# Kernel tuning notes

Hardware: AMD Instinct MI355X
Metric: run time of the kernel (lower is better)

## Reference

```python
import jax, jax.numpy as jnp
import numpy as np

B, T, D, DIM = 32, 2048, 1024, 1024


def setup_inputs() -> dict:
    key = jax.random.key(0)
    ks = jax.random.split(key, 7)
    def glorot(k, shape):
        lim = np.sqrt(6.0 / (shape[0] + shape[1]))
        return jax.random.uniform(k, shape, jnp.float32, -lim, lim)
    return {
        "input_states": jax.random.normal(ks[0], (B, T, D), jnp.float32),
        "last_state": jax.random.normal(ks[1], (B, D), jnp.float32),
        "Wy": glorot(ks[2], (D, DIM)),
        "Wh": glorot(ks[3], (D, DIM)),
        "w": glorot(ks[4], (DIM, 1)),
        "Wp": glorot(ks[5], (D, DIM)),
        "Wx": glorot(ks[6], (D, DIM)),
    }


def reference(input_states, last_state, Wy, Wh, w, Wp, Wx):
    # hs: (B,T,dim); last_state projection broadcast over T (the original
    # tiles last_state via a ones-matmul; a plain broadcast is the same math)
    hs = jnp.einsum("btd,de->bte", input_states, Wy)
    hproj = last_state @ Wh                      # (B,dim)
    m = jax.nn.relu(hs + hproj[:, None, :])      # (B,T,dim)
    scores = jnp.einsum("bte,eo->bt", m, w[:, :1])  # squeeze last dim
    alpha = jax.nn.softmax(scores, axis=-1)      # (B,T)
    r = jnp.einsum("bt,btd->bd", alpha, input_states)
    out = jax.nn.relu(r @ Wp + last_state @ Wx)  # (B,dim)
    return out
```

## Files before the change

kernel.cpp:

```cpp
#include <hip/hip_runtime.h>
#include <hip/hip_bf16.h>
#include <stdint.h>

#define BB 32
#define TT 2048
#define DD 1024
#define DIMQ 1024
#define MTOT (BB*TT)

typedef __attribute__((ext_vector_type(8))) __bf16 bf16x8;
typedef __attribute__((ext_vector_type(4))) float f32x4;

__device__ __forceinline__ unsigned short f2bf(float f) {
    unsigned int u = __float_as_uint(f);
    u += 0x7FFF + ((u >> 16) & 1);
    return (unsigned short)(u >> 16);
}
__device__ __forceinline__ float bf2f(unsigned short s) {
    return __uint_as_float(((unsigned int)s) << 16);
}

__device__ __forceinline__ void load_lds16(const void* g, void* l) {
    __builtin_amdgcn_global_load_lds(
        (const __attribute__((address_space(1))) unsigned int*)g,
        (__attribute__((address_space(3))) unsigned int*)l,
        16, 0, 0);
}

__global__ void cast_x(const float* __restrict__ x, unsigned short* __restrict__ xb) {
    long i = ((long)blockIdx.x * blockDim.x + threadIdx.x) * 4;
    float4 a = *(const float4*)(x + i);
    ushort4 o;
    o.x = f2bf(a.x); o.y = f2bf(a.y); o.z = f2bf(a.z); o.w = f2bf(a.w);
    *(ushort4*)(xb + i) = o;
}

__global__ void transpose_cast(const float* __restrict__ Wsrc, unsigned short* __restrict__ Wdst) {
    __shared__ float tile[32][33];
    int bx = blockIdx.x * 32;
    int by = blockIdx.y * 32;
    int tx = threadIdx.x & 31;
    int ty4 = (threadIdx.x >> 5) * 4;
    #pragma unroll
    for (int r = 0; r < 4; r++)
        tile[ty4 + r][tx] = Wsrc[(size_t)(by + ty4 + r) * DIMQ + bx + tx];
    __syncthreads();
    #pragma unroll
    for (int r = 0; r < 4; r++)
        Wdst[(size_t)(bx + ty4 + r) * DD + by + tx] = f2bf(tile[tx][ty4 + r]);
}

__global__ void vecmat2(const float* __restrict__ last,
                        const float* __restrict__ Wh, const float* __restrict__ Wx,
                        float* __restrict__ hproj, float* __restrict__ lsWx) {
    __shared__ float vs[DD];
    __shared__ float red[4][64];
    int b = blockIdx.y;
    int e0 = blockIdx.x * 64;
    const float* Mat = blockIdx.z ? Wx : Wh;
    float* outp = blockIdx.z ? lsWx : hproj;
    int tid = threadIdx.x;
    for (int d = tid; d < DD; d += 256) vs[d] = last[b * DD + d];
    __syncthreads();
    int e = tid & 63, dg = tid >> 6;
    int d0 = dg * 256;
    const float* Mp = Mat + (size_t)d0 * DIMQ + e0 + e;
    float acc = 0.f;
    #pragma unroll 8
    for (int d = 0; d < 256; d++) acc += vs[d0 + d] * Mp[(size_t)d * DIMQ];
    red[dg][e] = acc;
    __syncthreads();
    if (dg == 0)
        outp[b * DIMQ + e0 + e] = red[0][e] + red[1][e] + red[2][e] + red[3][e];
}

__global__ __launch_bounds__(512, 2)
void gemm_scores(const unsigned short* __restrict__ Xb,
                 const unsigned short* __restrict__ WyT,
                 const float* __restrict__ hproj,
                 const float* __restrict__ wvec,
                 float* __restrict__ partials) {
    __shared__ unsigned short lds[65536];
    __shared__ float lp[256];

    int tid = threadIdx.x;
    int lane = tid & 63;
    int wave = tid >> 6;
    int wr = wave >> 2;
    int wc = wave & 3;

    int bidx = blockIdx.x;
    int rr = bidx & 255, rnd = bidx >> 8;
    int xcd = rr & 7, slot = rr >> 3;
    int ntile = slot & 3;
    int mtile = rnd * 64 + xcd * 8 + (slot >> 2);

    if (tid < 256) lp[tid] = 0.f;

    int ssub = wave >> 1, sks = wave & 1;
    const unsigned short* aG = Xb  + (size_t)(mtile * 256 + ssub * 16 + (lane & 15)) * DD + sks * 32 + (lane >> 4) * 8;
    const unsigned short* bG = WyT + (size_t)(ntile * 256 + ssub * 16 + (lane & 15)) * DD + sks * 32 + (lane >> 4) * 8;
    unsigned short* ldsAst = &lds[(ssub * 128 + sks * 64 + lane) * 8];
    unsigned short* ldsBst = ldsAst + 16384;

    const unsigned short* aRd = &lds[wr * 8192 + lane * 8];
    const unsigned short* bRd = &lds[16384 + (wc >> 1) * 8192 + (wc & 1) * 4096 + lane * 8];

#define STAGE_A(S_, H_, T_) { \
    const unsigned short* g_ = aG + (size_t)(H_) * 131072 + (T_) * 64; \
    load_lds16(g_,         ldsAst + (S_) * 32768 + (H_) * 8192);       \
    load_lds16(g_ + 65536, ldsAst + (S_) * 32768 + (H_) * 8192 + 4096); }
#define STAGE_B(S_, H_, T_) { \
    const unsigned short* g_ = bG + (size_t)(H_) * 131072 + (T_) * 64; \
    load_lds16(g_,         ldsBst + (S_) * 32768 + (H_) * 8192);       \
    load_lds16(g_ + 65536, ldsBst + (S_) * 32768 + (H_) * 8192 + 4096); }
#define STAGE_TILE(S_, T_) { STAGE_A(S_, 0, T_); STAGE_A(S_, 1, T_); \
                             STAGE_B(S_, 0, T_); STAGE_B(S_, 1, T_); }

    f32x4 acc[8][4] = {};
    bf16x8 af[4][2], bfr[4][2];

#define LDA(S_, MH) { \
    _Pragma("unroll") for (int i_ = 0; i_ < 4; i_++) \
    _Pragma("unroll") for (int k_ = 0; k_ < 2; k_++) \
        af[i_][k_] = *reinterpret_cast<const bf16x8*>(aRd + (S_) * 32768 + ((MH) * 4 + i_) * 1024 + k_ * 512); }
#define LDB(S_, NH) { \
    _Pragma("unroll") for (int j_ = 0; j_ < 2; j_++) \
    _Pragma("unroll") for (int k_ = 0; k_ < 2; k_++) \
        bfr[(NH) * 2 + j_][k_] = *reinterpret_cast<const bf16x8*>(bRd + (S_) * 32768 + ((NH) * 2 + j_) * 1024 + k_ * 512); }
#define MFMA_Q(MH, NH) { \
    _Pragma("unroll") for (int k_ = 0; k_ < 2; k_++) \
    _Pragma("unroll") for (int i_ = 0; i_ < 4; i_++) \
    _Pragma("unroll") for (int j_ = 0; j_ < 2; j_++) \
        acc[(MH) * 4 + i_][(NH) * 2 + j_] = __builtin_amdgcn_mfma_f32_16x16x32_bf16( \
            af[i_][k_], bfr[(NH) * 2 + j_][k_], acc[(MH) * 4 + i_][(NH) * 2 + j_], 0, 0, 0); }

#define BAR() __builtin_amdgcn_s_barrier()
#define LGKM0() asm volatile("s_waitcnt lgkmcnt(0)" ::: "memory")
#define VMW8() asm volatile("s_waitcnt vmcnt(8)" ::: "memory")
#define PRIO1() __builtin_amdgcn_s_setprio(1)
#define PRIO0() __builtin_amdgcn_s_setprio(0)

    STAGE_TILE(0, 0);
    STAGE_TILE(1, 1);

    #pragma unroll 2
    for (int t = 0; t < 16; ++t) {
        int s = t & 1;
        int tp = (t + 2 > 15) ? 15 : (t + 2);

        VMW8();
        BAR();

        LDB(s, 0); LDB(s, 1);
        LDA(s, 0);
        PRIO1(); MFMA_Q(0, 0); MFMA_Q(0, 1); PRIO0();

        LDA(s, 1);
        LGKM0();
        BAR();

        STAGE_TILE(s, tp);
        PRIO1(); MFMA_Q(1, 0); MFMA_Q(1, 1); PRIO0();
    }

    __syncthreads();

    int bIdx = mtile >> 3;
    int q = lane >> 4, l15 = lane & 15;

    float hpv[4], wvv[4];
    #pragma unroll
    for (int nf = 0; nf < 4; nf++) {
        int n = ntile * 256 + wc * 64 + nf * 16 + l15;
        hpv[nf] = hproj[bIdx * DIMQ + n];
        wvv[nf] = wvec[n];
    }

    #pragma unroll
    for (int m = 0; m < 8; m++) {
        f32x4 s = {0.f, 0.f, 0.f, 0.f};
        #pragma unroll
        for (int nf = 0; nf < 4; nf++) {
            #pragma unroll
            for (int r = 0; r < 4; r++) {
                float v = acc[m][nf][r] + hpv[nf];
                v = v > 0.f ? v : 0.f;
                s[r] += v * wvv[nf];
            }
        }
        #pragma unroll
        for (int off = 1; off < 16; off <<= 1) {
            s[0] += __shfl_xor(s[0], off);
            s[1] += __shfl_xor(s[1], off);
            s[2] += __shfl_xor(s[2], off);
            s[3] += __shfl_xor(s[3], off);
        }
        if (l15 == 0) {
            int mrow = wr * 128 + m * 16 + q * 4;
            atomicAdd(&lp[mrow + 0], s[0]);
            atomicAdd(&lp[mrow + 1], s[1]);
            atomicAdd(&lp[mrow + 2], s[2]);
            atomicAdd(&lp[mrow + 3], s[3]);
        }
    }
    __syncthreads();
    if (tid < 256)
        partials[(size_t)ntile * MTOT + mtile * 256 + tid] = lp[tid];

#undef STAGE_A
#undef STAGE_B
#undef STAGE_TILE
#undef LDA
#undef LDB
#undef MFMA_Q
#undef BAR
#undef LGKM0
#undef VMW8
#undef PRIO1
#undef PRIO0
}

__global__ void softmax_alpha(const float* __restrict__ partials, float* __restrict__ alpha) {
    __shared__ float wred[4];
    __shared__ float wsum[4];
    int b = blockIdx.x;
    int tid = threadIdx.x;
    float s[8];
    float mx = -1e30f;
    #pragma unroll
    for (int c = 0; c < 8; c++) {
        int t = b * TT + tid + c * 256;
        float v = 0.f;
        #pragma unroll
        for (int p = 0; p < 4; p++) v += partials[(size_t)p * MTOT + t];
        s[c] = v;
        mx = fmaxf(mx, v);
    }
    for (int off = 32; off; off >>= 1) mx = fmaxf(mx, __shfl_xor(mx, off));
    if ((tid & 63) == 0) wred[tid >> 6] = mx;
    __syncthreads();
    mx = fmaxf(fmaxf(wred[0], wred[1]), fmaxf(wred[2], wred[3]));
    float sum = 0.f;
    #pragma unroll
    for (int c = 0; c < 8; c++) { s[c] = expf(s[c] - mx); sum += s[c]; }
    for (int off = 32; off; off >>= 1) sum += __shfl_xor(sum, off);
    if ((tid & 63) == 0) wsum[tid >> 6] = sum;
    __syncthreads();
    sum = wsum[0] + wsum[1] + wsum[2] + wsum[3];
    float inv = 1.f / sum;
    #pragma unroll
    for (int c = 0; c < 8; c++) alpha[b * TT + tid + c * 256] = s[c] * inv;
}

__global__ void weighted_sum(const unsigned short* __restrict__ Xb,
                             const float* __restrict__ alpha,
                             float* __restrict__ r_part) {
    __shared__ float al[128];
    int tc = blockIdx.x, b = blockIdx.y, tid = threadIdx.x;
    if (tid < 128) al[tid] = alpha[b * TT + tc * 128 + tid];
    __syncthreads();
    int d0 = tid * 4;
    const unsigned short* base = Xb + ((size_t)(b * TT + tc * 128)) * DD + d0;
    f32x4 acc = {0.f, 0.f, 0.f, 0.f};
    #pragma unroll 2
    for (int t = 0; t < 128; t++) {
        ushort4 xv = *(const ushort4*)(base + (size_t)t * DD);
        float a_ = al[t];
        acc[0] += a_ * bf2f(xv.x);
        acc[1] += a_ * bf2f(xv.y);
        acc[2] += a_ * bf2f(xv.z);
        acc[3] += a_ * bf2f(xv.w);
    }
    float* o = r_part + ((size_t)tc * BB + b) * DD + d0;
    *(float4*)o = *(float4*)&acc;
}

__global__ void final_out(const float* __restrict__ r_part, const float* __restrict__ Wp,
                          const float* __restrict__ lsWx, float* __restrict__ out) {
    __shared__ float rs[DD];
    __shared__ float red[4][64];
    int b = blockIdx.y;
    int e0 = blockIdx.x * 64;
    int tid = threadIdx.x;
    for (int d = tid; d < DD; d += 256) {
        float v = 0.f;
        #pragma unroll
        for (int p = 0; p < 16; p++) v += r_part[((size_t)p * BB + b) * DD + d];
        rs[d] = v;
    }
    __syncthreads();
    int e = tid & 63, dg = tid >> 6;
    int d0 = dg * 256;
    const float* Mp = Wp + (size_t)d0 * DIMQ + e0 + e;
    float acc = 0.f;
    #pragma unroll 8
    for (int d = 0; d < 256; d++) acc += rs[d0 + d] * Mp[(size_t)d * DIMQ];
    red[dg][e] = acc;
    __syncthreads();
    if (dg == 0) {
        float v = red[0][e] + red[1][e] + red[2][e] + red[3][e]
                + lsWx[b * DIMQ + e0 + e];
        out[b * DIMQ + e0 + e] = fmaxf(v, 0.f);
    }
}

extern "C" void kernel_launch(void* const* d_in, const int* in_sizes, int n_in,
                              void* d_out, int out_size, void* d_ws, size_t ws_size,
                              hipStream_t stream) {
    const float* x    = (const float*)d_in[0];
    const float* last = (const float*)d_in[1];
    const float* Wy   = (const float*)d_in[2];
    const float* Wh   = (const float*)d_in[3];
    const float* w    = (const float*)d_in[4];
    const float* Wp   = (const float*)d_in[5];
    const float* Wx   = (const float*)d_in[6];
    float* out = (float*)d_out;

    char* ws = (char*)d_ws;
    unsigned short* Xb   = (unsigned short*)(ws);
    unsigned short* WyT  = (unsigned short*)(ws + 134217728);
    float* hproj         = (float*)(ws + 136314880);
    float* lsWx          = (float*)(ws + 136445952);
    float* partials      = (float*)(ws + 136577024);
    float* alpha         = (float*)(ws + 137625600);
    float* r_part        = (float*)(ws + 137887744);

    cast_x<<<BB*TT*DD/4/256, 256, 0, stream>>>(x, Xb);
    transpose_cast<<<dim3(32, 32), 256, 0, stream>>>(Wy, WyT);
    vecmat2<<<dim3(DIMQ/64, BB, 2), 256, 0, stream>>>(last, Wh, Wx, hproj, lsWx);
    gemm_scores<<<1024, 512, 0, stream>>>(Xb, WyT, hproj, w, partials);
    softmax_alpha<<<BB, 256, 0, stream>>>(partials, alpha);
    weighted_sum<<<dim3(TT/128, BB), 256, 0, stream>>>(Xb, alpha, r_part);
    final_out<<<dim3(DIMQ/64, BB), 256, 0, stream>>>(r_part, Wp, lsWx, out);
}
```

Baseline: 621.8 us.

## Fuse fp32-to-bf16 cast of X into GEMM A-tile staging via registers

After: 667.7 us. +7.4%, slower.

```diff
diff --git a/kernel.cpp b/kernel.cpp
--- a/kernel.cpp
+++ b/kernel.cpp
@@ -16,23 +16,12 @@
     u += 0x7FFF + ((u >> 16) & 1);
     return (unsigned short)(u >> 16);
 }
-__device__ __forceinline__ float bf2f(unsigned short s) {
-    return __uint_as_float(((unsigned int)s) << 16);
-}
 
 __device__ __forceinline__ void load_lds16(const void* g, void* l) {
     __builtin_amdgcn_global_load_lds(
         (const __attribute__((address_space(1))) unsigned int*)g,
         (__attribute__((address_space(3))) unsigned int*)l,
         16, 0, 0);
-}
-
-__global__ void cast_x(const float* __restrict__ x, unsigned short* __restrict__ xb) {
-    long i = ((long)blockIdx.x * blockDim.x + threadIdx.x) * 4;
-    float4 a = *(const float4*)(x + i);
-    ushort4 o;
-    o.x = f2bf(a.x); o.y = f2bf(a.y); o.z = f2bf(a.z); o.w = f2bf(a.w);
-    *(ushort4*)(xb + i) = o;
 }
 
 __global__ void transpose_cast(const float* __restrict__ Wsrc, unsigned short* __restrict__ Wdst) {
@@ -75,7 +64,7 @@
 }
 
 __global__ __launch_bounds__(512, 2)
-void gemm_scores(const unsigned short* __restrict__ Xb,
+void gemm_scores(const float* __restrict__ Xf,
                  const unsigned short* __restrict__ WyT,
                  const float* __restrict__ hproj,
                  const float* __restrict__ wvec,
@@ -98,24 +87,42 @@
     if (tid < 256) lp[tid] = 0.f;
 
     int ssub = wave >> 1, sks = wave & 1;
-    const unsigned short* aG = Xb  + (size_t)(mtile * 256 + ssub * 16 + (lane & 15)) * DD + sks * 32 + (lane >> 4) * 8;
-    const unsigned short* bG = WyT + (size_t)(ntile * 256 + ssub * 16 + (lane & 15)) * DD + sks * 32 + (lane >> 4) * 8;
+    const float* aF = Xf + (size_t)(mtile * 256 + ssub * 16 + (lane & 15)) * DD
+                    + sks * 32 + (lane >> 4) * 8;
+    const unsigned short* bG = WyT + (size_t)(ntile * 256 + ssub * 16 + (lane & 15)) * DD
+                             + sks * 32 + (lane >> 4) * 8;
     unsigned short* ldsAst = &lds[(ssub * 128 + sks * 64 + lane) * 8];
     unsigned short* ldsBst = ldsAst + 16384;
 
     const unsigned short* aRd = &lds[wr * 8192 + lane * 8];
     const unsigned short* bRd = &lds[16384 + (wc >> 1) * 8192 + (wc & 1) * 4096 + lane * 8];
 
-#define STAGE_A(S_, H_, T_) { \
-    const unsigned short* g_ = aG + (size_t)(H_) * 131072 + (T_) * 64; \
-    load_lds16(g_,         ldsAst + (S_) * 32768 + (H_) * 8192);       \
-    load_lds16(g_ + 65536, ldsAst + (S_) * 32768 + (H_) * 8192 + 4096); }
-#define STAGE_B(S_, H_, T_) { \
-    const unsigned short* g_ = bG + (size_t)(H_) * 131072 + (T_) * 64; \
-    load_lds16(g_,         ldsBst + (S_) * 32768 + (H_) * 8192);       \
-    load_lds16(g_ + 65536, ldsBst + (S_) * 32768 + (H_) * 8192 + 4096); }
-#define STAGE_TILE(S_, T_) { STAGE_A(S_, 0, T_); STAGE_A(S_, 1, T_); \
-                             STAGE_B(S_, 0, T_); STAGE_B(S_, 1, T_); }
+    float4 rA0[8], rA1[8];
+
+#define AISSUE(RS, T_) { \
+    _Pragma("unroll") for (int q_ = 0; q_ < 8; q_++) { \
+        int H_ = q_ >> 2, p_ = (q_ >> 1) & 1, h_ = q_ & 1; \
+        RS[q_] = *reinterpret_cast<const float4*>( \
+            aF + (size_t)(H_ * 128 + p_ * 64) * DD + (T_) * 64 + h_ * 4); } }
+
+#define AWRITE(RS, S_) { \
+    _Pragma("unroll") for (int c_ = 0; c_ < 4; c_++) { \
+        unsigned int u0_, u1_, u2_, u3_; \
+        asm volatile("v_cvt_pk_bf16_f32 %0, %1, %2" : "=v"(u0_) : "v"(RS[c_*2].x),   "v"(RS[c_*2].y)); \
+        asm volatile("v_cvt_pk_bf16_f32 %0, %1, %2" : "=v"(u1_) : "v"(RS[c_*2].z),   "v"(RS[c_*2].w)); \
+        asm volatile("v_cvt_pk_bf16_f32 %0, %1, %2" : "=v"(u2_) : "v"(RS[c_*2+1].x), "v"(RS[c_*2+1].y)); \
+        asm volatile("v_cvt_pk_bf16_f32 %0, %1, %2" : "=v"(u3_) : "v"(RS[c_*2+1].z), "v"(RS[c_*2+1].w)); \
+        uint4 pk_; pk_.x = u0_; pk_.y = u1_; pk_.z = u2_; pk_.w = u3_; \
+        int H_ = c_ >> 1, p_ = c_ & 1; \
+        *reinterpret_cast<uint4*>(ldsAst + (S_) * 32768 + H_ * 8192 + p_ * 4096) = pk_; } }
+
+#define BSTAGE(S_, T_) { \
+    { const unsigned short* g_ = bG + (T_) * 64; \
+      load_lds16(g_,         ldsBst + (S_) * 32768); \
+      load_lds16(g_ + 65536, ldsBst + (S_) * 32768 + 4096); } \
+    { const unsigned short* g_ = bG + (size_t)131072 + (T_) * 64; \
+      load_lds16(g_,         ldsBst + (S_) * 32768 + 8192); \
+      load_lds16(g_ + 65536, ldsBst + (S_) * 32768 + 8192 + 4096); } }
 
     f32x4 acc[8][4] = {};
     bf16x8 af[4][2], bfr[4][2];
@@ -137,31 +144,39 @@
 
 #define BAR() __builtin_amdgcn_s_barrier()
 #define LGKM0() asm volatile("s_waitcnt lgkmcnt(0)" ::: "memory")
-#define VMW8() asm volatile("s_waitcnt vmcnt(8)" ::: "memory")
+#define VMW12() asm volatile("s_waitcnt vmcnt(12)" ::: "memory")
 #define PRIO1() __builtin_amdgcn_s_setprio(1)
 #define PRIO0() __builtin_amdgcn_s_setprio(0)
 
-    STAGE_TILE(0, 0);
-    STAGE_TILE(1, 1);
-
-    #pragma unroll 2
-    for (int t = 0; t < 16; ++t) {
-        int s = t & 1;
-        int tp = (t + 2 > 15) ? 15 : (t + 2);
-
-        VMW8();
-        BAR();
-
-        LDB(s, 0); LDB(s, 1);
-        LDA(s, 0);
-        PRIO1(); MFMA_Q(0, 0); MFMA_Q(0, 1); PRIO0();
-
-        LDA(s, 1);
-        LGKM0();
-        BAR();
-
-        STAGE_TILE(s, tp);
-        PRIO1(); MFMA_Q(1, 0); MFMA_Q(1, 1); PRIO0();
+    AISSUE(rA0, 0);
+    AISSUE(rA1, 1);
+    AWRITE(rA0, 0);
+    BSTAGE(0, 0);
+    AWRITE(rA1, 1);
+    AISSUE(rA0, 2);
+    BSTAGE(1, 1);
+    LGKM0();
+
+#define ITER(T_, SA_, SB_) { \
+    const int s_ = (T_) & 1; \
+    int tpa_ = (T_) + 3; if (tpa_ > 15) tpa_ = 15; \
+    int tpb_ = (T_) + 2; if (tpb_ > 15) tpb_ = 15; \
+    VMW12();             \
+    BAR();               \
+    LDB(s_, 0); LDB(s_, 1); \
+    LDA(s_, 0); \
+    PRIO1(); MFMA_Q(0, 0); MFMA_Q(0, 1); PRIO0(); \
+    LDA(s_, 1); \
+    LGKM0();             \
+    BAR();               \
+    AWRITE(SA_, s_);     \
+    AISSUE(SB_, tpa_);   \
+    BSTAGE(s_, tpb_);    \
+    PRIO1(); MFMA_Q(1, 0); MFMA_Q(1, 1); PRIO0(); }
+
+    for (int tt = 0; tt < 8; ++tt) {
+        ITER(2 * tt,     rA0, rA1);
+        ITER(2 * tt + 1, rA1, rA0);
     }
 
     __syncthreads();
@@ -208,17 +223,18 @@
     if (tid < 256)
         partials[(size_t)ntile * MTOT + mtile * 256 + tid] = lp[tid];
 
-#undef STAGE_A
-#undef STAGE_B
-#undef STAGE_TILE
+#undef AISSUE
+#undef AWRITE
+#undef BSTAGE
 #undef LDA
 #undef LDB
 #undef MFMA_Q
 #undef BAR
 #undef LGKM0
-#undef VMW8
+#undef VMW12
 #undef PRIO1
 #undef PRIO0
+#undef ITER
 }
 
 __global__ void softmax_alpha(const float* __restrict__ partials, float* __restrict__ alpha) {
@@ -253,7 +269,7 @@
     for (int c = 0; c < 8; c++) alpha[b * TT + tid + c * 256] = s[c] * inv;
 }
 
-__global__ void weighted_sum(const unsigned short* __restrict__ Xb,
+__global__ void weighted_sum(const float* __restrict__ Xf,
                              const float* __restrict__ alpha,
                              float* __restrict__ r_part) {
     __shared__ float al[128];
@@ -261,16 +277,16 @@
     if (tid < 128) al[tid] = alpha[b * TT + tc * 128 + tid];
     __syncthreads();
     int d0 = tid * 4;
-    const unsigned short* base = Xb + ((size_t)(b * TT + tc * 128)) * DD + d0;
+    const float* base = Xf + ((size_t)(b * TT + tc * 128)) * DD + d0;
     f32x4 acc = {0.f, 0.f, 0.f, 0.f};
     #pragma unroll 2
     for (int t = 0; t < 128; t++) {
-        ushort4 xv = *(const ushort4*)(base + (size_t)t * DD);
+        float4 xv = *(const float4*)(base + (size_t)t * DD);
         float a_ = al[t];
-        acc[0] += a_ * bf2f(xv.x);
-        acc[1] += a_ * bf2f(xv.y);
-        acc[2] += a_ * bf2f(xv.z);
-        acc[3] += a_ * bf2f(xv.w);
+        acc[0] += a_ * xv.x;
+        acc[1] += a_ * xv.y;
+        acc[2] += a_ * xv.z;
+        acc[3] += a_ * xv.w;
     }
     float* o = r_part + ((size_t)tc * BB + b) * DD + d0;
     *(float4*)o = *(float4*)&acc;
@@ -318,7 +334,6 @@
     float* out = (float*)d_out;
 
     char* ws = (char*)d_ws;
-    unsigned short* Xb   = (unsigned short*)(ws);
     unsigned short* WyT  = (unsigned short*)(ws + 134217728);
     float* hproj         = (float*)(ws + 136314880);
     float* lsWx          = (float*)(ws + 136445952);
@@ -326,11 +341,10 @@
     float* alpha         = (float*)(ws + 137625600);
     float* r_part        = (float*)(ws + 137887744);
 
-    cast_x<<<BB*TT*DD/4/256, 256, 0, stream>>>(x, Xb);
     transpose_cast<<<dim3(32, 32), 256, 0, stream>>>(Wy, WyT);
     vecmat2<<<dim3(DIMQ/64, BB, 2), 256, 0, stream>>>(last, Wh, Wx, hproj, lsWx);
-    gemm_scores<<<1024, 512, 0, stream>>>(Xb, WyT, hproj, w, partials);
+    gemm_scores<<<1024, 512, 0, stream>>>(x, WyT, hproj, w, partials);
     softmax_alpha<<<BB, 256, 0, stream>>>(partials, alpha);
-    weighted_sum<<<dim3(TT/128, BB), 256, 0, stream>>>(Xb, alpha, r_part);
+    weighted_sum<<<dim3(TT/128, BB), 256, 0, stream>>>(x, alpha, r_part);
     final_out<<<dim3(DIMQ/64, BB), 256, 0, stream>>>(r_part, Wp, lsWx, out);
 }
```
